# Optimization experiments

Measured on AMD Instinct MI355X. Metric: run time of the kernel, lower is better.

## Reference

```python
import jax, jax.numpy as jnp
import numpy as np

SIZE = 1024      # codebook size
DIM = 64         # latent_dim
TOPK = 3
BETA_C = 0.25
LEGACY = False

def setup_inputs() -> dict:
    key = jax.random.key(0)
    kz, ke = jax.random.split(key)
    z = jax.random.normal(kz, (16, 64, 64, DIM), dtype=jnp.float32)
    # nn.Embedding init: uniform(-1/size, 1/size)
    emb = jax.random.uniform(ke, (SIZE, DIM), minval=-1.0 / SIZE, maxval=1.0 / SIZE, dtype=jnp.float32)
    return {"z": z, "emb": emb}

def reference(z, emb):
    zf = z.reshape(-1, DIM)                                  # [N, D]
    # squared euclidean distances via matmul expansion: [N, SIZE]
    d = (jnp.sum(zf ** 2, axis=1, keepdims=True)
         + jnp.sum(emb ** 2, axis=1)
         - 2.0 * (zf @ emb.T))
    neg_d, topk_idx = jax.lax.top_k(-d, TOPK)                # smallest distances -> [N, K]
    # direct gather instead of one-hot matmul (same math)
    z_q = jnp.mean(emb[topk_idx], axis=1).reshape(z.shape)   # [N,K,D] -> [N,D] -> z.shape
    if LEGACY:
        loss = (jnp.mean((jax.lax.stop_gradient(z_q) - z) ** 2)
                + BETA_C * jnp.mean((z_q - jax.lax.stop_gradient(z)) ** 2))
    else:
        loss = (BETA_C * jnp.mean((jax.lax.stop_gradient(z_q) - z) ** 2)
                + jnp.mean((z_q - jax.lax.stop_gradient(z)) ** 2))
    # one-hot encodings are part of the module's return signature
    topk_encodings = jax.nn.one_hot(topk_idx, SIZE, dtype=z.dtype)   # [N, K, SIZE]
    e_mean = jnp.mean(topk_encodings, axis=(0, 1))                   # [SIZE]
    perplexity = jnp.exp(-jnp.sum(e_mean * jnp.log(e_mean + 1e-10)))
    z_q_st = z + jax.lax.stop_gradient(z_q - z)              # straight-through estimator
    return (z_q_st, loss, perplexity, topk_encodings, topk_idx)
```

## Files before the change

### kernel.cpp

```cpp
#include <hip/hip_runtime.h>
#include <math.h>

#define N_ROWS 65536
#define CB 1024
#define SPLITS 4
#define JS (CB / SPLITS)

typedef float v4f __attribute__((ext_vector_type(4)));

__device__ __forceinline__ float tree_sum64_sq(const float* x) {
#pragma clang fp contract(off)
    float sq[64];
#pragma unroll
    for (int i = 0; i < 64; ++i) sq[i] = x[i] * x[i];
    float s[16];
#pragma unroll
    for (int l = 0; l < 16; ++l) s[l] = (sq[l] + sq[l + 16]) + (sq[l + 32] + sq[l + 48]);
    float t[8];
#pragma unroll
    for (int l = 0; l < 8; ++l) t[l] = s[l] + s[l + 8];
    float u[4];
#pragma unroll
    for (int l = 0; l < 4; ++l) u[l] = t[l] + t[l + 4];
    float v0 = u[0] + u[2];
    float v1 = u[1] + u[3];
    return v0 + v1;
}

__device__ __forceinline__ void top3_insert(float d, int j,
                                            float& v0, float& v1, float& v2,
                                            int& i0, int& i1, int& i2) {
    bool b0 = d < v0, b1 = d < v1, b2 = d < v2;
    v2 = b1 ? v1 : (b2 ? d : v2);
    i2 = b1 ? i1 : (b2 ? j : i2);
    v1 = b0 ? v0 : (b1 ? d : v1);
    i1 = b0 ? i0 : (b1 ? j : i1);
    v0 = b0 ? d : v0;
    i0 = b0 ? j : i0;
}

__global__ __launch_bounds__(256) void prep_kernel(const float* __restrict__ emb,
                                                   float* __restrict__ B,
                                                   int* __restrict__ hist,
                                                   float* __restrict__ lossAcc) {
    int j = blockIdx.x * 256 + threadIdx.x;
    if (j >= CB) return;
    float e[64];
    const float4* e4 = (const float4*)(emb + (size_t)j * 64);
#pragma unroll
    for (int k = 0; k < 16; ++k) {
        float4 v = e4[k];
        e[4 * k] = v.x; e[4 * k + 1] = v.y; e[4 * k + 2] = v.z; e[4 * k + 3] = v.w;
    }
    B[j] = tree_sum64_sq(e);
    hist[j] = 0;
    if (j == 0) *lossAcc = 0.0f;
}

__global__ __launch_bounds__(256) void fused_kernel(const float* __restrict__ z,
                                                    const float* __restrict__ emb,
                                                    const float* __restrict__ B,
                                                    float* __restrict__ out0,
                                                    float* __restrict__ out3f,
                                                    float* __restrict__ out4,
                                                    int* __restrict__ hist,
                                                    float* __restrict__ lossAcc) {
    __shared__ float sD[SPLITS][64][3];
    __shared__ int   sI[SPLITS][64][3];
    __shared__ int   topk_lds[192];

    int t = threadIdx.x;
    int r = t & 63;
    int split = __builtin_amdgcn_readfirstlane(t >> 6);
    int row = blockIdx.x * 64 + r;

    float zr[64];
    const float4* z4 = (const float4*)(z + (size_t)row * 64);
#pragma unroll
    for (int k = 0; k < 16; ++k) {
        float4 v = z4[k];
        zr[4 * k] = v.x; zr[4 * k + 1] = v.y; zr[4 * k + 2] = v.z; zr[4 * k + 3] = v.w;
    }
    float A = tree_sum64_sq(zr);

    float v0 = 3.402823466e38f, v1 = 3.402823466e38f, v2 = 3.402823466e38f;
    int i0 = 0, i1 = 0, i2 = 0;
    int jbase = split * JS;

#pragma unroll 2
    for (int jj = 0; jj < JS; ++jj) {
        int j = jbase + jj;
        const float4* e4 = (const float4*)(emb + (size_t)j * 64);
        float Bj = B[j];
        float acc = 0.0f;
#pragma unroll
        for (int k = 0; k < 16; ++k) {
            float4 e = e4[k];
            acc = fmaf(zr[4 * k],     e.x, acc);
            acc = fmaf(zr[4 * k + 1], e.y, acc);
            acc = fmaf(zr[4 * k + 2], e.z, acc);
            acc = fmaf(zr[4 * k + 3], e.w, acc);
        }
        float d = (A + Bj) - 2.0f * acc;
        top3_insert(d, j, v0, v1, v2, i0, i1, i2);
    }

    sD[split][r][0] = v0; sD[split][r][1] = v1; sD[split][r][2] = v2;
    sI[split][r][0] = i0; sI[split][r][1] = i1; sI[split][r][2] = i2;
    __syncthreads();

    if (t < 64) {
        float m0 = 3.402823466e38f, m1 = 3.402823466e38f, m2 = 3.402823466e38f;
        int j0 = 0, j1 = 0, j2 = 0;
#pragma unroll
        for (int s = 0; s < SPLITS; ++s) {
#pragma unroll
            for (int u = 0; u < 3; ++u)
                top3_insert(sD[s][r][u], sI[s][r][u], m0, m1, m2, j0, j1, j2);
        }

        topk_lds[r * 3]     = j0;
        topk_lds[r * 3 + 1] = j1;
        topk_lds[r * 3 + 2] = j2;

        const float4* e0q = (const float4*)(emb + (size_t)j0 * 64);
        const float4* e1q = (const float4*)(emb + (size_t)j1 * 64);
        const float4* e2q = (const float4*)(emb + (size_t)j2 * 64);
        v4f* o4 = (v4f*)(out0 + (size_t)row * 64);

        float lsum = 0.0f;
#pragma unroll
        for (int k4 = 0; k4 < 16; ++k4) {
            float4 a = e0q[k4], b = e1q[k4], c = e2q[k4];
            float zx = zr[4 * k4], zy = zr[4 * k4 + 1];
            float zz = zr[4 * k4 + 2], zw = zr[4 * k4 + 3];
            v4f st;
            float zq, df;
            zq = ((a.x + b.x) + c.x) / 3.0f; df = zq - zx; st.x = zx + df; lsum = fmaf(df, df, lsum);
            zq = ((a.y + b.y) + c.y) / 3.0f; df = zq - zy; st.y = zy + df; lsum = fmaf(df, df, lsum);
            zq = ((a.z + b.z) + c.z) / 3.0f; df = zq - zz; st.z = zz + df; lsum = fmaf(df, df, lsum);
            zq = ((a.w + b.w) + c.w) / 3.0f; df = zq - zw; st.w = zw + df; lsum = fmaf(df, df, lsum);
            __builtin_nontemporal_store(st, o4 + k4);
        }

        size_t ob = (size_t)row * 3;
        out4[ob]     = (float)j0;
        out4[ob + 1] = (float)j1;
        out4[ob + 2] = (float)j2;
        atomicAdd(&hist[j0], 1);
        atomicAdd(&hist[j1], 1);
        atomicAdd(&hist[j2], 1);

#pragma unroll
        for (int off = 32; off >= 1; off >>= 1) lsum += __shfl_down(lsum, off);
        if ((t & 63) == 0) atomicAdd(lossAcc, lsum);
    }
    __syncthreads();

    float* Rb = out3f + (size_t)blockIdx.x * 196608;
    v4f* R4 = (v4f*)(Rb + 2);
    const int M = (196608 - 2) / 4;

    for (int m = t; m < M; m += 256) {
        int e  = 2 + 4 * m;
        int s0 = e >> 10;
        int c  = e & 1023;
        int s3 = (e + 3) >> 10;
        int ia = topk_lds[s0];
        int ib = topk_lds[s3];
        v4f v;
        v.x = (c     == ia) ? 1.0f : 0.0f;
        v.y = (c + 1 == ia) ? 1.0f : 0.0f;
        v.z = (((c + 2) & 1023) == ib) ? 1.0f : 0.0f;
        v.w = (((c + 3) & 1023) == ib) ? 1.0f : 0.0f;
        __builtin_nontemporal_store(v, R4 + m);
    }
    if (t == 0) {
        int ia = topk_lds[0];
        Rb[0] = (ia == 0) ? 1.0f : 0.0f;
        Rb[1] = (ia == 1) ? 1.0f : 0.0f;
        int ib = topk_lds[191];
        Rb[196606] = (ib == 1022) ? 1.0f : 0.0f;
        Rb[196607] = (ib == 1023) ? 1.0f : 0.0f;
    }
}

__global__ __launch_bounds__(256) void finalize_kernel(const int* __restrict__ hist,
                                                       const float* __restrict__ lossAcc,
                                                       float* __restrict__ out1,
                                                       float* __restrict__ out2) {
    __shared__ float red[256];
    int t = threadIdx.x;
    float local = 0.0f;
    for (int b = t; b < CB; b += 256) {
        float em = (float)hist[b] / 196608.0f;
        local += em * logf(em + 1e-10f);
    }
    red[t] = local;
    __syncthreads();
    for (int s = 128; s >= 1; s >>= 1) {
        if (t < s) red[t] += red[t + s];
        __syncthreads();
    }
    if (t == 0) {
        *out2 = expf(-red[0]);
        float m = *lossAcc / 4194304.0f;
        *out1 = 0.25f * m + m;
    }
}

extern "C" void kernel_launch(void* const* d_in, const int* in_sizes, int n_in,
                              void* d_out, int out_size, void* d_ws, size_t ws_size,
                              hipStream_t stream) {
    const float* z   = (const float*)d_in[0];
    const float* emb = (const float*)d_in[1];

    float* out  = (float*)d_out;
    float* out0 = out;
    float* out1 = out + 4194304;
    float* out2 = out + 4194305;
    float* out3 = out + 4194306;
    float* out4 = out + 4194306 + 201326592ll;

    int*   hist    = (int*)d_ws;
    float* lossAcc = (float*)((char*)d_ws + 4096);
    float* B       = (float*)((char*)d_ws + 8192);

    prep_kernel<<<4, 256, 0, stream>>>(emb, B, hist, lossAcc);
    fused_kernel<<<N_ROWS / 64, 256, 0, stream>>>(z, emb, B, out0, out3, out4,
                                                  hist, lossAcc);
    finalize_kernel<<<1, 256, 0, stream>>>(hist, lossAcc, out1, out2);
}
```

Baseline: 1.061 ms.

## Interleave one-hot zero-fill into distance loop and scatter ones afterward

Rather than writing the large one-hot encoding tensor in a separate phase after top-k selection, each thread issues zero-fill stores for its block's slice during the codebook distance loop. After the merge, it scatters the three 1.0 entries per row. The aim is to overlap the heavy memory-write traffic with the compute-bound dot-product loop and remove the post-sync write phase. In exchange, the zero stores and the later ones depend on the barrier for ordering within the block. The stores also switch from nontemporal to regular, which may pollute caches and add pressure inside the hot loop.

```diff
diff --git a/kernel.cpp b/kernel.cpp
--- a/kernel.cpp
+++ b/kernel.cpp
@@ -67,13 +67,20 @@
                                                     float* __restrict__ lossAcc) {
     __shared__ float sD[SPLITS][64][3];
     __shared__ int   sI[SPLITS][64][3];
-    __shared__ int   topk_lds[192];
 
     int t = threadIdx.x;
     int r = t & 63;
     int split = __builtin_amdgcn_readfirstlane(t >> 6);
     int row = blockIdx.x * 64 + r;
 
+    float* Rb = out3f + (size_t)blockIdx.x * 196608;
+    v4f* R4 = (v4f*)(Rb + 2);
+    if (t == 0) {
+        Rb[0] = 0.0f; Rb[1] = 0.0f;
+        Rb[196606] = 0.0f; Rb[196607] = 0.0f;
+    }
+    v4f zero4 = {0.0f, 0.0f, 0.0f, 0.0f};
+
     float zr[64];
     const float4* z4 = (const float4*)(z + (size_t)row * 64);
 #pragma unroll
@@ -89,6 +96,10 @@
 
 #pragma unroll 2
     for (int jj = 0; jj < JS; ++jj) {
+        if (jj < 192) {
+            int m = jj * 256 + t;
+            if (m < 49151) R4[m] = zero4;
+        }
         int j = jbase + jj;
         const float4* e4 = (const float4*)(emb + (size_t)j * 64);
         float Bj = B[j];
@@ -119,9 +130,9 @@
                 top3_insert(sD[s][r][u], sI[s][r][u], m0, m1, m2, j0, j1, j2);
         }
 
-        topk_lds[r * 3]     = j0;
-        topk_lds[r * 3 + 1] = j1;
-        topk_lds[r * 3 + 2] = j2;
+        Rb[(r * 3    ) * 1024 + j0] = 1.0f;
+        Rb[(r * 3 + 1) * 1024 + j1] = 1.0f;
+        Rb[(r * 3 + 2) * 1024 + j2] = 1.0f;
 
         const float4* e0q = (const float4*)(emb + (size_t)j0 * 64);
         const float4* e1q = (const float4*)(emb + (size_t)j1 * 64);
@@ -140,7 +151,7 @@
             zq = ((a.y + b.y) + c.y) / 3.0f; df = zq - zy; st.y = zy + df; lsum = fmaf(df, df, lsum);
             zq = ((a.z + b.z) + c.z) / 3.0f; df = zq - zz; st.z = zz + df; lsum = fmaf(df, df, lsum);
             zq = ((a.w + b.w) + c.w) / 3.0f; df = zq - zw; st.w = zw + df; lsum = fmaf(df, df, lsum);
-            __builtin_nontemporal_store(st, o4 + k4);
+            o4[k4] = st;
         }
 
         size_t ob = (size_t)row * 3;
@@ -154,34 +165,6 @@
 #pragma unroll
         for (int off = 32; off >= 1; off >>= 1) lsum += __shfl_down(lsum, off);
         if ((t & 63) == 0) atomicAdd(lossAcc, lsum);
-    }
-    __syncthreads();
-
-    float* Rb = out3f + (size_t)blockIdx.x * 196608;
-    v4f* R4 = (v4f*)(Rb + 2);
-    const int M = (196608 - 2) / 4;
-
-    for (int m = t; m < M; m += 256) {
-        int e  = 2 + 4 * m;
-        int s0 = e >> 10;
-        int c  = e & 1023;
-        int s3 = (e + 3) >> 10;
-        int ia = topk_lds[s0];
-        int ib = topk_lds[s3];
-        v4f v;
-        v.x = (c     == ia) ? 1.0f : 0.0f;
-        v.y = (c + 1 == ia) ? 1.0f : 0.0f;
-        v.z = (((c + 2) & 1023) == ib) ? 1.0f : 0.0f;
-        v.w = (((c + 3) & 1023) == ib) ? 1.0f : 0.0f;
-        __builtin_nontemporal_store(v, R4 + m);
-    }
-    if (t == 0) {
-        int ia = topk_lds[0];
-        Rb[0] = (ia == 0) ? 1.0f : 0.0f;
-        Rb[1] = (ia == 1) ? 1.0f : 0.0f;
-        int ib = topk_lds[191];
-        Rb[196606] = (ib == 1022) ? 1.0f : 0.0f;
-        Rb[196607] = (ib == 1023) ? 1.0f : 0.0f;
     }
 }
 
```

Result: no change. 1.081 ms (+1.9%).
